# Optimization experiments

Measured on AMD Instinct MI355X. Metric: run time of the kernel, lower is better.

The kernel has to match this reference:

```python
import jax, jax.numpy as jnp
import numpy as np

DIM = 1024
N_HEAD = 16
HEAD_DIM = DIM // N_HEAD
SCALE = HEAD_DIM ** (-0.5)


def setup_inputs() -> dict:
    key = jax.random.key(0)
    ks = jax.random.split(key, 5)
    x = jax.random.normal(ks[0], (2, 2048, DIM), dtype=jnp.float32)
    # Linear params (torch nn.Linear stores weight as [out, in]; we keep [in, out])
    wqkv = jax.random.normal(ks[1], (DIM, 3 * DIM), dtype=jnp.float32) / np.sqrt(DIM)
    bqkv = jax.random.normal(ks[2], (3 * DIM,), dtype=jnp.float32) * 0.01
    wo = jax.random.normal(ks[3], (DIM, DIM), dtype=jnp.float32) / np.sqrt(DIM)
    bo = jax.random.normal(ks[4], (DIM,), dtype=jnp.float32) * 0.01
    return {"x": x, "wqkv": wqkv, "bqkv": bqkv, "wo": wo, "bo": bo}


def reference(x, wqkv, bqkv, wo, bo):
    b, s, _ = x.shape
    qkv = x @ wqkv + bqkv                      # [b, s, 3*dim]
    q, k, v = jnp.split(qkv, 3, axis=-1)
    # [b, s, h, d] -> [b, h, s, d]
    def heads(t):
        return t.reshape(b, s, N_HEAD, HEAD_DIM).transpose(0, 2, 1, 3)
    q, k, v = heads(q) * SCALE, heads(k), heads(v)
    attn = jnp.einsum('bhqd,bhkd->bhqk', q, k)  # [b, h, s, s]
    attn = jax.nn.softmax(attn, axis=-1)
    out = jnp.einsum('bhqk,bhkd->bhqd', attn, v)
    out = out.transpose(0, 2, 1, 3).reshape(b, s, DIM)
    return out @ wo + bo
```

## Files before the change

kernel.cpp:

```cpp
#include <hip/hip_runtime.h>
#include <hip/hip_bf16.h>

#define DIM   1024
#define NHEAD 16
#define HDIM  64
#define BATCH 2
#define SEQ   2048
#define TOK   (BATCH*SEQ)
#define QSCALE 0.1803368801111204f

typedef unsigned short u16;
typedef __attribute__((ext_vector_type(8))) _Float16 h16x8;
typedef __attribute__((ext_vector_type(2))) __fp16 fp16x2;
typedef __attribute__((ext_vector_type(4))) float f32x4;
typedef __attribute__((ext_vector_type(16))) float f32x16;
typedef __attribute__((ext_vector_type(2))) int i32x2;

__device__ __forceinline__ u16 f2h(float f) {
    union { _Float16 h; u16 u; } v; v.h = (_Float16)f;
    return v.u;
}
__device__ __forceinline__ unsigned pack2h(float a, float b) {
    return (unsigned)f2h(a) | ((unsigned)f2h(b) << 16);
}
__device__ __forceinline__ unsigned pkrtz(float a, float b) {
    union { fp16x2 h; unsigned u; } v;
    v.h = __builtin_amdgcn_cvt_pkrtz(a, b);
    return v.u;
}
__device__ __forceinline__ f32x16 zero16() {
    f32x16 v;
#pragma unroll
    for (int i = 0; i < 16; ++i) v[i] = 0.f;
    return v;
}

typedef __attribute__((address_space(3))) void lds_void;
typedef const __attribute__((address_space(1))) void gbl_void;
__device__ __forceinline__ void gload_lds16(const void* g, void* l) {
    __builtin_amdgcn_global_load_lds((gbl_void*)g, (lds_void*)l, 16, 0, 0);
}

__global__ __launch_bounds__(256)
void cvt_f16(const float* __restrict__ in, u16* __restrict__ out) {
    int i = blockIdx.x * 256 + threadIdx.x;
    float4 v = ((const float4*)in)[i];
    ((uint2*)out)[i] = make_uint2(pack2h(v.x, v.y), pack2h(v.z, v.w));
}

__global__ __launch_bounds__(256)
void cvt_f16_T(const float* __restrict__ in, u16* __restrict__ outT,
               int K, int N) {
    __shared__ float t[32][33];
    const int n0 = blockIdx.x * 32, k0 = blockIdx.y * 32;
    const int tx = threadIdx.x & 31, ty = threadIdx.x >> 5;
#pragma unroll
    for (int i = 0; i < 4; ++i)
        t[ty + i * 8][tx] = in[(size_t)(k0 + ty + i * 8) * N + n0 + tx];
    __syncthreads();
#pragma unroll
    for (int i = 0; i < 4; ++i)
        outT[(size_t)(n0 + ty + i * 8) * K + k0 + tx] = f2h(t[tx][ty + i * 8]);
}

__global__ __launch_bounds__(256)
void gemm_qkv(const u16* __restrict__ Ag, const u16* __restrict__ Bg,
              const float* __restrict__ bias, u16* __restrict__ Qh,
              u16* __restrict__ Kh, u16* __restrict__ Vh, int K, int N) {
    __shared__ u16 As[128 * 64];
    __shared__ u16 Bs[128 * 64];

    const int tid  = threadIdx.x;
    const int lane = tid & 63;
    const int w    = tid >> 6;
    const int c    = lane & 15;
    const int quad = lane >> 4;
    const int wm   = (w & 1) * 64;
    const int wn   = (w >> 1) * 64;
    const int row0 = blockIdx.y * 128;
    const int col0 = blockIdx.x * 128;
    const int sw   = c & 7;

    f32x4 acc[4][4];
#pragma unroll
    for (int m = 0; m < 4; ++m)
#pragma unroll
        for (int n = 0; n < 4; ++n) acc[m][n] = (f32x4){0.f, 0.f, 0.f, 0.f};

    for (int k0 = 0; k0 < K; k0 += 64) {
        __syncthreads();
#pragma unroll
        for (int i = 0; i < 4; ++i) {
            int idx = tid + i * 256;
            int r = idx >> 3, p = idx & 7;
            int g = p ^ (r & 7);
            gload_lds16(Ag + (size_t)(row0 + r) * K + k0 + g * 8, &As[idx * 8]);
            gload_lds16(Bg + (size_t)(col0 + r) * K + k0 + g * 8, &Bs[idx * 8]);
        }
        __syncthreads();

        h16x8 af[4][2];
#pragma unroll
        for (int m = 0; m < 4; ++m)
#pragma unroll
            for (int kh = 0; kh < 2; ++kh)
                af[m][kh] = *(const h16x8*)&As[(wm + m * 16 + c) * 64 +
                                              ((kh * 4 + quad) ^ sw) * 8];
#pragma unroll
        for (int kh = 0; kh < 2; ++kh)
#pragma unroll
            for (int n = 0; n < 4; ++n) {
                h16x8 bf = *(const h16x8*)&Bs[(wn + n * 16 + c) * 64 +
                                              ((kh * 4 + quad) ^ sw) * 8];
#pragma unroll
                for (int m = 0; m < 4; ++m)
                    acc[m][n] = __builtin_amdgcn_mfma_f32_16x16x32_f16(
                        af[m][kh], bf, acc[m][n], 0, 0, 0);
            }
    }

#pragma unroll
    for (int n = 0; n < 4; ++n) {
        const int col = col0 + wn + n * 16 + c;
        const float bv = bias[col];
        const int h = (col >> 6) & 15, d = col & 63;
#pragma unroll
        for (int m = 0; m < 4; ++m) {
            const int rbase = row0 + wm + m * 16 + quad * 4;
            const int b = rbase >> 11, s0 = rbase & (SEQ - 1);
            const int bh = (b << 4) + h;
            if (col0 < DIM) {
#pragma unroll
                for (int r = 0; r < 4; ++r)
                    Qh[((size_t)bh * SEQ + s0 + r) * 64 + d] =
                        f2h((acc[m][n][r] + bv) * QSCALE);
            } else if (col0 < 2 * DIM) {
#pragma unroll
                for (int r = 0; r < 4; ++r)
                    Kh[((size_t)bh * SEQ + s0 + r) * 64 + d] =
                        f2h(acc[m][n][r] + bv);
            } else {
                uint2 pv = make_uint2(pack2h(acc[m][n][0] + bv, acc[m][n][1] + bv),
                                      pack2h(acc[m][n][2] + bv, acc[m][n][3] + bv));
                *(uint2*)&Vh[((size_t)bh * 64 + d) * SEQ + s0] = pv;
            }
        }
    }
}

__global__ __launch_bounds__(256)
void gemm_out(const u16* __restrict__ Ag, const u16* __restrict__ Bg,
              const float* __restrict__ bias, float* __restrict__ Cout,
              int M, int N, int K) {
    __shared__ u16 As[128 * 64];
    __shared__ u16 Bs[64 * 64];

    const int tid  = threadIdx.x;
    const int lane = tid & 63;
    const int w    = tid >> 6;
    const int c    = lane & 15;
    const int quad = lane >> 4;
    const int wm   = w * 32;
    const int row0 = blockIdx.y * 128;
    const int col0 = blockIdx.x * 64;
    const int sw   = c & 7;

    f32x4 acc[2][4];
#pragma unroll
    for (int m = 0; m < 2; ++m)
#pragma unroll
        for (int n = 0; n < 4; ++n) acc[m][n] = (f32x4){0.f, 0.f, 0.f, 0.f};

    for (int k0 = 0; k0 < K; k0 += 64) {
        __syncthreads();
#pragma unroll
        for (int i = 0; i < 4; ++i) {
            int idx = tid + i * 256;
            int r = idx >> 3, p = idx & 7;
            int g = p ^ (r & 7);
            gload_lds16(Ag + (size_t)(row0 + r) * K + k0 + g * 8, &As[idx * 8]);
        }
#pragma unroll
        for (int i = 0; i < 2; ++i) {
            int idx = tid + i * 256;
            int r = idx >> 3, p = idx & 7;
            int g = p ^ (r & 7);
            gload_lds16(Bg + (size_t)(col0 + r) * K + k0 + g * 8, &Bs[idx * 8]);
        }
        __syncthreads();

        h16x8 af[2][2];
#pragma unroll
        for (int m = 0; m < 2; ++m)
#pragma unroll
            for (int kh = 0; kh < 2; ++kh)
                af[m][kh] = *(const h16x8*)&As[(wm + m * 16 + c) * 64 +
                                              ((kh * 4 + quad) ^ sw) * 8];
#pragma unroll
        for (int kh = 0; kh < 2; ++kh)
#pragma unroll
            for (int n = 0; n < 4; ++n) {
                h16x8 bf = *(const h16x8*)&Bs[(n * 16 + c) * 64 +
                                              ((kh * 4 + quad) ^ sw) * 8];
#pragma unroll
                for (int m = 0; m < 2; ++m)
                    acc[m][n] = __builtin_amdgcn_mfma_f32_16x16x32_f16(
                        af[m][kh], bf, acc[m][n], 0, 0, 0);
            }
    }

#pragma unroll
    for (int n = 0; n < 4; ++n) {
        const int col = col0 + n * 16 + c;
        const float bv = bias[col];
#pragma unroll
        for (int m = 0; m < 2; ++m) {
            const int rbase = row0 + wm + m * 16 + quad * 4;
#pragma unroll
            for (int r = 0; r < 4; ++r)
                Cout[(size_t)(rbase + r) * N + col] = acc[m][n][r] + bv;
        }
    }
}

__global__ __launch_bounds__(256)
void flash_attn8(const u16* __restrict__ Qg, const u16* __restrict__ Kg,
                 const u16* __restrict__ Vg, u16* __restrict__ aout) {
    __shared__ u16 Qs[128 * 64];
    __shared__ u16 Ks[2][128 * 64];
    __shared__ u16 Vt[2][64 * 128];

    const int tid  = threadIdx.x;
    const int lane = tid & 63;
    const int w    = tid >> 6;
    const int n32  = lane & 31;
    const int q5   = lane >> 5;
    const int bh   = blockIdx.y;
    const int q0   = blockIdx.x * 128;

    const u16* Qb = Qg + (size_t)bh * SEQ * 64;
    const u16* Kb = Kg + (size_t)bh * SEQ * 64;
    const u16* Vb = Vg + (size_t)bh * 64 * SEQ;

#pragma unroll
    for (int i = 0; i < 4; ++i) {
        int idx = tid + i * 256;
        int r = idx >> 3, p = idx & 7, g = p ^ (r & 7);
        gload_lds16(Qb + (size_t)(q0 + r) * 64 + g * 8, &Qs[idx * 8]);
    }
#pragma unroll
    for (int i = 0; i < 4; ++i) {
        int idx = tid + i * 256;
        int rk = idx >> 3, pk = idx & 7, gk = pk ^ (rk & 7);
        gload_lds16(Kb + (size_t)rk * 64 + gk * 8, &Ks[0][idx * 8]);
        int rv = idx >> 4, cv = idx & 15, gv = cv ^ (rv & 7);
        gload_lds16(Vb + (size_t)rv * SEQ + gv * 8, &Vt[0][idx * 8]);
    }
    __syncthreads();

    const int qrow = w * 32 + n32;
    const int sw   = n32 & 7;
    h16x8 qb[4];
#pragma unroll
    for (int s = 0; s < 4; ++s)
        qb[s] = *(const h16x8*)&Qs[qrow * 64 + (((s * 2 + q5) ^ sw) * 8)];

    float l = 0.f;
    f32x16 o[2] = {zero16(), zero16()};

    for (int kt = 0; kt < SEQ / 128; ++kt) {
        const int cur = kt & 1, nxt = cur ^ 1;

        if (kt < SEQ / 128 - 1) {
            const int k1 = (kt + 1) * 128;
#pragma unroll
            for (int i = 0; i < 4; ++i) {
                int idx = tid + i * 256;
                int rk = idx >> 3, pk = idx & 7, gk = pk ^ (rk & 7);
                gload_lds16(Kb + (size_t)(k1 + rk) * 64 + gk * 8, &Ks[nxt][idx * 8]);
                int rv = idx >> 4, cv = idx & 15, gv = cv ^ (rv & 7);
                gload_lds16(Vb + (size_t)rv * SEQ + k1 + gv * 8, &Vt[nxt][idx * 8]);
            }
        }

#pragma unroll
        for (int sub2 = 0; sub2 < 2; ++sub2) {
            unsigned xw[8][2];
#pragma unroll
            for (int sub = 0; sub < 2; ++sub) {
                const int kr = sub2 * 64 + sub * 32 + n32;
                f32x16 sa = zero16();
                __builtin_amdgcn_s_setprio(1);
#pragma unroll
                for (int s = 0; s < 4; ++s) {
                    h16x8 ak = *(const h16x8*)&Ks[cur][kr * 64 +
                                                       (((s * 2 + q5) ^ sw) * 8)];
                    sa = __builtin_amdgcn_mfma_f32_32x32x16_f16(ak, qb[s], sa, 0, 0, 0);
                }
                __builtin_amdgcn_s_setprio(0);
#pragma unroll
                for (int rr = 0; rr < 4; ++rr) {
                    float p0 = __builtin_amdgcn_exp2f(sa[4 * rr + 0]);
                    float p1 = __builtin_amdgcn_exp2f(sa[4 * rr + 1]);
                    float p2 = __builtin_amdgcn_exp2f(sa[4 * rr + 2]);
                    float p3 = __builtin_amdgcn_exp2f(sa[4 * rr + 3]);
                    l += (p0 + p1) + (p2 + p3);
                    xw[sub * 4 + rr][0] = pkrtz(p0, p1);
                    xw[sub * 4 + rr][1] = pkrtz(p2, p3);
                }
            }

            h16x8 bp[4];
#pragma unroll
            for (int s = 0; s < 4; ++s) {
                i32x2 ra = __builtin_amdgcn_permlane32_swap(
                    (int)xw[2 * s][0], (int)xw[2 * s + 1][0], false, false);
                i32x2 rb = __builtin_amdgcn_permlane32_swap(
                    (int)xw[2 * s][1], (int)xw[2 * s + 1][1], false, false);
                union { int u[4]; h16x8 h; } f;
                f.u[0] = ra[0];
                f.u[1] = rb[0];
                f.u[2] = ra[1];
                f.u[3] = rb[1];
                bp[s] = f.h;
            }

            __builtin_amdgcn_s_setprio(1);
#pragma unroll
            for (int dt = 0; dt < 2; ++dt) {
                const int dr = dt * 32 + n32;
#pragma unroll
                for (int s = 0; s < 4; ++s) {
                    h16x8 av = *(const h16x8*)&Vt[cur][dr * 128 +
                                                       ((sub2 * 8 + ((s * 2 + q5) ^ sw)) * 8)];
                    o[dt] = __builtin_amdgcn_mfma_f32_32x32x16_f16(av, bp[s], o[dt], 0, 0, 0);
                }
            }
            __builtin_amdgcn_s_setprio(0);
        }

        __syncthreads();
    }

    l += __shfl_xor(l, 32, 64);
    const float inv = 1.f / l;

    const int b = bh >> 4, h = bh & 15;
    const size_t ro = (size_t)(b * SEQ + q0 + qrow) * DIM + h * HDIM;
#pragma unroll
    for (int dt = 0; dt < 2; ++dt) {
#pragma unroll
        for (int rq = 0; rq < 4; ++rq) {
            const int d = dt * 32 + 8 * rq + 4 * q5;
            *(uint2*)&aout[ro + d] = make_uint2(
                pkrtz(o[dt][4 * rq + 0] * inv, o[dt][4 * rq + 1] * inv),
                pkrtz(o[dt][4 * rq + 2] * inv, o[dt][4 * rq + 3] * inv));
        }
    }
}

extern "C" void kernel_launch(void* const* d_in, const int* in_sizes, int n_in,
                              void* d_out, int out_size, void* d_ws, size_t ws_size,
                              hipStream_t stream) {
    (void)in_sizes; (void)n_in; (void)out_size; (void)ws_size;
    const float* x    = (const float*)d_in[0];
    const float* wqkv = (const float*)d_in[1];
    const float* bqkv = (const float*)d_in[2];
    const float* wo   = (const float*)d_in[3];
    const float* bo   = (const float*)d_in[4];
    float* out = (float*)d_out;

    const size_t HB = (size_t)BATCH * NHEAD * SEQ * HDIM;
    u16* Qh  = (u16*)d_ws;
    u16* Kh  = Qh + HB;
    u16* Vh  = Kh + HB;
    u16* ao  = Vh + HB;
    u16* wqT = ao + (size_t)TOK * DIM;
    u16* woT = wqT + (size_t)3 * DIM * DIM;
    u16* xh  = woT + (size_t)DIM * DIM;

    cvt_f16<<<TOK * DIM / 4 / 256, 256, 0, stream>>>(x, xh);
    cvt_f16_T<<<dim3(3 * DIM / 32, DIM / 32), 256, 0, stream>>>(wqkv, wqT, DIM, 3 * DIM);
    cvt_f16_T<<<dim3(DIM / 32, DIM / 32), 256, 0, stream>>>(wo, woT, DIM, DIM);
    gemm_qkv<<<dim3(3 * DIM / 128, TOK / 128), 256, 0, stream>>>(
        xh, wqT, bqkv, Qh, Kh, Vh, DIM, 3 * DIM);
    flash_attn8<<<dim3(SEQ / 128, BATCH * NHEAD), 256, 0, stream>>>(
        Qh, Kh, Vh, ao);
    gemm_out<<<dim3(DIM / 64, TOK / 128), 256, 0, stream>>>(
        ao, woT, bo, out, TOK, DIM, DIM);
}
```

Measured before the change: 191.1 us.

## Split attention key tiles across two wave groups with LDS reduction

```diff
diff --git a/kernel.cpp b/kernel.cpp
--- a/kernel.cpp
+++ b/kernel.cpp
@@ -223,9 +223,9 @@
     }
 }
 
-__global__ __launch_bounds__(256)
-void flash_attn8(const u16* __restrict__ Qg, const u16* __restrict__ Kg,
-                 const u16* __restrict__ Vg, u16* __restrict__ aout) {
+__global__ __launch_bounds__(512, 4)
+void flash_attn10(const u16* __restrict__ Qg, const u16* __restrict__ Kg,
+                  const u16* __restrict__ Vg, u16* __restrict__ aout) {
     __shared__ u16 Qs[128 * 64];
     __shared__ u16 Ks[2][128 * 64];
     __shared__ u16 Vt[2][64 * 128];
@@ -233,6 +233,8 @@
     const int tid  = threadIdx.x;
     const int lane = tid & 63;
     const int w    = tid >> 6;
+    const int wq   = w & 3;
+    const int wk   = w >> 2;
     const int n32  = lane & 31;
     const int q5   = lane >> 5;
     const int bh   = blockIdx.y;
@@ -243,14 +245,14 @@
     const u16* Vb = Vg + (size_t)bh * 64 * SEQ;
 
 #pragma unroll
-    for (int i = 0; i < 4; ++i) {
-        int idx = tid + i * 256;
+    for (int i = 0; i < 2; ++i) {
+        int idx = tid + i * 512;
         int r = idx >> 3, p = idx & 7, g = p ^ (r & 7);
         gload_lds16(Qb + (size_t)(q0 + r) * 64 + g * 8, &Qs[idx * 8]);
     }
 #pragma unroll
-    for (int i = 0; i < 4; ++i) {
-        int idx = tid + i * 256;
+    for (int i = 0; i < 2; ++i) {
+        int idx = tid + i * 512;
         int rk = idx >> 3, pk = idx & 7, gk = pk ^ (rk & 7);
         gload_lds16(Kb + (size_t)rk * 64 + gk * 8, &Ks[0][idx * 8]);
         int rv = idx >> 4, cv = idx & 15, gv = cv ^ (rv & 7);
@@ -258,7 +260,7 @@
     }
     __syncthreads();
 
-    const int qrow = w * 32 + n32;
+    const int qrow = wq * 32 + n32;
     const int sw   = n32 & 7;
     h16x8 qb[4];
 #pragma unroll
@@ -274,8 +276,8 @@
         if (kt < SEQ / 128 - 1) {
             const int k1 = (kt + 1) * 128;
 #pragma unroll
-            for (int i = 0; i < 4; ++i) {
-                int idx = tid + i * 256;
+            for (int i = 0; i < 2; ++i) {
+                int idx = tid + i * 512;
                 int rk = idx >> 3, pk = idx & 7, gk = pk ^ (rk & 7);
                 gload_lds16(Kb + (size_t)(k1 + rk) * 64 + gk * 8, &Ks[nxt][idx * 8]);
                 int rv = idx >> 4, cv = idx & 15, gv = cv ^ (rv & 7);
@@ -283,68 +285,85 @@
             }
         }
 
-#pragma unroll
-        for (int sub2 = 0; sub2 < 2; ++sub2) {
-            unsigned xw[8][2];
-#pragma unroll
-            for (int sub = 0; sub < 2; ++sub) {
-                const int kr = sub2 * 64 + sub * 32 + n32;
-                f32x16 sa = zero16();
-                __builtin_amdgcn_s_setprio(1);
-#pragma unroll
-                for (int s = 0; s < 4; ++s) {
-                    h16x8 ak = *(const h16x8*)&Ks[cur][kr * 64 +
-                                                       (((s * 2 + q5) ^ sw) * 8)];
-                    sa = __builtin_amdgcn_mfma_f32_32x32x16_f16(ak, qb[s], sa, 0, 0, 0);
-                }
-                __builtin_amdgcn_s_setprio(0);
-#pragma unroll
-                for (int rr = 0; rr < 4; ++rr) {
-                    float p0 = __builtin_amdgcn_exp2f(sa[4 * rr + 0]);
-                    float p1 = __builtin_amdgcn_exp2f(sa[4 * rr + 1]);
-                    float p2 = __builtin_amdgcn_exp2f(sa[4 * rr + 2]);
-                    float p3 = __builtin_amdgcn_exp2f(sa[4 * rr + 3]);
-                    l += (p0 + p1) + (p2 + p3);
-                    xw[sub * 4 + rr][0] = pkrtz(p0, p1);
-                    xw[sub * 4 + rr][1] = pkrtz(p2, p3);
-                }
-            }
-
-            h16x8 bp[4];
+        unsigned xw[8][2];
+#pragma unroll
+        for (int sub = 0; sub < 2; ++sub) {
+            const int kr = wk * 64 + sub * 32 + n32;
+            f32x16 sa = zero16();
+            __builtin_amdgcn_s_setprio(1);
 #pragma unroll
             for (int s = 0; s < 4; ++s) {
-                i32x2 ra = __builtin_amdgcn_permlane32_swap(
-                    (int)xw[2 * s][0], (int)xw[2 * s + 1][0], false, false);
-                i32x2 rb = __builtin_amdgcn_permlane32_swap(
-                    (int)xw[2 * s][1], (int)xw[2 * s + 1][1], false, false);
-                union { int u[4]; h16x8 h; } f;
-                f.u[0] = ra[0];
-                f.u[1] = rb[0];
-                f.u[2] = ra[1];
-                f.u[3] = rb[1];
-                bp[s] = f.h;
-            }
-
-            __builtin_amdgcn_s_setprio(1);
-#pragma unroll
-            for (int dt = 0; dt < 2; ++dt) {
-                const int dr = dt * 32 + n32;
-#pragma unroll
-                for (int s = 0; s < 4; ++s) {
-                    h16x8 av = *(const h16x8*)&Vt[cur][dr * 128 +
-                                                       ((sub2 * 8 + ((s * 2 + q5) ^ sw)) * 8)];
-                    o[dt] = __builtin_amdgcn_mfma_f32_32x32x16_f16(av, bp[s], o[dt], 0, 0, 0);
-                }
+                h16x8 ak = *(const h16x8*)&Ks[cur][kr * 64 +
+                                                   (((s * 2 + q5) ^ sw) * 8)];
+                sa = __builtin_amdgcn_mfma_f32_32x32x16_f16(ak, qb[s], sa, 0, 0, 0);
             }
             __builtin_amdgcn_s_setprio(0);
-        }
+#pragma unroll
+            for (int rr = 0; rr < 4; ++rr) {
+                float p0 = __builtin_amdgcn_exp2f(sa[4 * rr + 0]);
+                float p1 = __builtin_amdgcn_exp2f(sa[4 * rr + 1]);
+                float p2 = __builtin_amdgcn_exp2f(sa[4 * rr + 2]);
+                float p3 = __builtin_amdgcn_exp2f(sa[4 * rr + 3]);
+                l += (p0 + p1) + (p2 + p3);
+                xw[sub * 4 + rr][0] = pkrtz(p0, p1);
+                xw[sub * 4 + rr][1] = pkrtz(p2, p3);
+            }
+        }
+
+        h16x8 bp[4];
+#pragma unroll
+        for (int s = 0; s < 4; ++s) {
+            i32x2 ra = __builtin_amdgcn_permlane32_swap(
+                (int)xw[2 * s][0], (int)xw[2 * s + 1][0], false, false);
+            i32x2 rb = __builtin_amdgcn_permlane32_swap(
+                (int)xw[2 * s][1], (int)xw[2 * s + 1][1], false, false);
+            union { int u[4]; h16x8 h; } f;
+            f.u[0] = ra[0];
+            f.u[1] = rb[0];
+            f.u[2] = ra[1];
+            f.u[3] = rb[1];
+            bp[s] = f.h;
+        }
+
+        __builtin_amdgcn_s_setprio(1);
+#pragma unroll
+        for (int dt = 0; dt < 2; ++dt) {
+            const int dr = dt * 32 + n32;
+#pragma unroll
+            for (int s = 0; s < 4; ++s) {
+                h16x8 av = *(const h16x8*)&Vt[cur][dr * 128 +
+                                                   ((wk * 8 + ((s * 2 + q5) ^ sw)) * 8)];
+                o[dt] = __builtin_amdgcn_mfma_f32_32x32x16_f16(av, bp[s], o[dt], 0, 0, 0);
+            }
+        }
+        __builtin_amdgcn_s_setprio(0);
 
         __syncthreads();
     }
 
     l += __shfl_xor(l, 32, 64);
+
+    float* oc = (float*)Vt;
+    float* lc = (float*)Qs;
+    const int orow = (wq * 64 + lane) * 32;
+    if (wk == 1) {
+#pragma unroll
+        for (int dt = 0; dt < 2; ++dt)
+#pragma unroll
+            for (int i = 0; i < 16; ++i)
+                oc[orow + ((dt * 16 + i + lane) & 31)] = o[dt][i];
+        lc[wq * 64 + lane] = l;
+    }
+    __syncthreads();
+    if (wk == 1) return;
+    l += lc[wq * 64 + lane];
+#pragma unroll
+    for (int dt = 0; dt < 2; ++dt)
+#pragma unroll
+        for (int i = 0; i < 16; ++i)
+            o[dt][i] += oc[orow + ((dt * 16 + i + lane) & 31)];
+
     const float inv = 1.f / l;
-
     const int b = bh >> 4, h = bh & 15;
     const size_t ro = (size_t)(b * SEQ + q0 + qrow) * DIM + h * HDIM;
 #pragma unroll
@@ -384,7 +403,7 @@
     cvt_f16_T<<<dim3(DIM / 32, DIM / 32), 256, 0, stream>>>(wo, woT, DIM, DIM);
     gemm_qkv<<<dim3(3 * DIM / 128, TOK / 128), 256, 0, stream>>>(
         xh, wqT, bqkv, Qh, Kh, Vh, DIM, 3 * DIM);
-    flash_attn8<<<dim3(SEQ / 128, BATCH * NHEAD), 256, 0, stream>>>(
+    flash_attn10<<<dim3(SEQ / 128, BATCH * NHEAD), 512, 0, stream>>>(
         Qh, Kh, Vh, ao);
     gemm_out<<<dim3(DIM / 64, TOK / 128), 256, 0, stream>>>(
         ao, woT, bo, out, TOK, DIM, DIM);
```

After: 185.5 us. 1.03x faster.
